# Kernel tuning notes

Measured on AMD Instinct MI355X. Metric: run time of the kernel, lower is better.

The kernel has to match this reference:

```python
import jax, jax.numpy as jnp
import numpy as np

DIM = 512
HEADS = 8
DIM_HEAD = 64
SCALE = DIM_HEAD ** -0.5


def setup_inputs() -> dict:
    key = jax.random.key(0)
    k1, k2, k3 = jax.random.split(key, 3)
    b, n = 2, 4096
    x = jax.random.normal(k1, (b, n, DIM), dtype=jnp.float32)
    ln_gamma = jnp.ones((DIM,), dtype=jnp.float32)
    ln_beta = jnp.zeros((DIM,), dtype=jnp.float32)
    w_qkv = jax.random.normal(k2, (DIM, 3 * HEADS * DIM_HEAD), dtype=jnp.float32) * (DIM ** -0.5)
    w_out = jax.random.normal(k3, (HEADS * DIM_HEAD, DIM), dtype=jnp.float32) * ((HEADS * DIM_HEAD) ** -0.5)
    b_out = jnp.zeros((DIM,), dtype=jnp.float32)
    return {"x": x, "ln_gamma": ln_gamma, "ln_beta": ln_beta,
            "w_qkv": w_qkv, "w_out": w_out, "b_out": b_out}


def reference(x, ln_gamma, ln_beta, w_qkv, w_out, b_out):
    # LayerNorm over last dim (eps matches torch default 1e-5)
    mu = jnp.mean(x, axis=-1, keepdims=True)
    var = jnp.mean(jnp.square(x - mu), axis=-1, keepdims=True)
    xn = (x - mu) * jax.lax.rsqrt(var + 1e-5) * ln_gamma + ln_beta

    b, n, _ = xn.shape
    qkv = xn @ w_qkv                                  # [b, n, 3*h*d]
    q, k, v = jnp.split(qkv, 3, axis=-1)
    # [b, n, h*d] -> [b, h, n, d]
    reshape = lambda t: t.reshape(b, n, HEADS, DIM_HEAD).transpose(0, 2, 1, 3)
    q, k, v = reshape(q), reshape(k), reshape(v)

    dots = jnp.einsum('bhid,bhjd->bhij', q, k) * SCALE  # [b, h, n, n]
    attn = jax.nn.softmax(dots, axis=-1)
    out = jnp.einsum('bhij,bhjd->bhid', attn, v)        # [b, h, n, d]
    out = out.transpose(0, 2, 1, 3).reshape(b, n, HEADS * DIM_HEAD)
    return out @ w_out + b_out
```

## Files before the change

kernel.cpp:

```cpp
#include <hip/hip_runtime.h>
#include <stdint.h>

#define NBATCH 2
#define NSEQ   4096
#define DIMF   512
#define HEADS  8
#define DHEAD  64
#define MTOK   (NBATCH*NSEQ)
#define NBH    (NBATCH*HEADS)

typedef __bf16 bf16x8 __attribute__((ext_vector_type(8)));
typedef float  f32x4  __attribute__((ext_vector_type(4)));
typedef short  short8v __attribute__((ext_vector_type(8)));

__device__ __forceinline__ unsigned short f2bf(float f) {
  unsigned x = __builtin_bit_cast(unsigned, f);
  x += 0x7fffu + ((x >> 16) & 1u);
  return (unsigned short)(x >> 16);
}

__device__ __forceinline__ void gld16(void* lds, const void* g) {
  __builtin_amdgcn_global_load_lds(
      (const __attribute__((address_space(1))) unsigned*)g,
      (__attribute__((address_space(3))) unsigned*)lds, 16, 0, 0);
}

__global__ __launch_bounds__(256) void ln_kernel(
    const float* __restrict__ x, const float* __restrict__ gamma,
    const float* __restrict__ beta, unsigned* __restrict__ xnb) {
  const int row = blockIdx.x;
  const int t = threadIdx.x;
  const float2 v = *(const float2*)(x + (size_t)row * DIMF + t * 2);
  float s1 = v.x + v.y;
  float s2 = v.x * v.x + v.y * v.y;
#pragma unroll
  for (int m = 1; m < 64; m <<= 1) { s1 += __shfl_xor(s1, m); s2 += __shfl_xor(s2, m); }
  __shared__ float ls1[4], ls2[4];
  const int w = t >> 6;
  if ((t & 63) == 0) { ls1[w] = s1; ls2[w] = s2; }
  __syncthreads();
  s1 = ls1[0] + ls1[1] + ls1[2] + ls1[3];
  s2 = ls2[0] + ls2[1] + ls2[2] + ls2[3];
  const float mu  = s1 * (1.0f / 512.0f);
  const float var = s2 * (1.0f / 512.0f) - mu * mu;
  const float rs  = 1.0f / sqrtf(var + 1e-5f);
  const float2 g2 = *(const float2*)(gamma + t * 2);
  const float2 b2 = *(const float2*)(beta + t * 2);
  const float a0 = (v.x - mu) * rs * g2.x + b2.x;
  const float a1 = (v.y - mu) * rs * g2.y + b2.y;
  xnb[(size_t)row * 256 + t] = (unsigned)f2bf(a0) | ((unsigned)f2bf(a1) << 16);
}

__global__ __launch_bounds__(256) void wprep_kernel(
    const float* __restrict__ wqkv, const float* __restrict__ wout,
    unsigned short* __restrict__ wqkvT, unsigned short* __restrict__ woT) {
  const int tid = blockIdx.x * 256 + threadIdx.x;
  if (tid < 512 * 1536) {
    const int c = tid % 1536, k = tid / 1536;
    wqkvT[c * 512 + k] = f2bf(wqkv[(size_t)k * 1536 + c]);
  } else {
    const int i = tid - 512 * 1536;
    const int c = i % 512, k = i / 512;
    woT[c * 512 + k] = f2bf(wout[(size_t)k * 512 + c]);
  }
}

template <int MODE>
__global__ __launch_bounds__(256, 2) void gemm_kernel(
    const unsigned short* __restrict__ A, const unsigned short* __restrict__ Bt,
    unsigned short* __restrict__ Qb, unsigned short* __restrict__ Kb,
    unsigned short* __restrict__ Vb,
    const float* __restrict__ bias, float* __restrict__ Cout, int Ncols) {
  __shared__ short Ab[2][128 * 32];
  __shared__ short Bb[2][128 * 32];
  const int tid = threadIdx.x;
  const int w = tid >> 6, l = tid & 63;
  const int g = l >> 4, c = l & 15;
  const int nbn = Ncols >> 7;
  const int mb = blockIdx.x / nbn, nb = blockIdx.x % nbn;
  const int m0 = mb * 128, n0 = nb * 128;
  const int wr = w >> 1, wc = w & 1;

  f32x4 acc[4][4] = {};

  auto STAGE = [&](int buf, int kt) {
    const int k0 = kt * 32;
#pragma unroll
    for (int j = 0; j < 2; ++j) {
      const int row = w * 32 + j * 16 + (l >> 2);
      const int gk = (l & 3) ^ ((row >> 1) & 3);
      gld16(&Ab[buf][(w * 32 + j * 16) * 32], A + (size_t)(m0 + row) * 512 + k0 + gk * 8);
      gld16(&Bb[buf][(w * 32 + j * 16) * 32], Bt + (size_t)(n0 + row) * 512 + k0 + gk * 8);
    }
  };

  STAGE(0, 0);
  __syncthreads();

  for (int kt = 0; kt < 16; ++kt) {
    const int buf = kt & 1;
    if (kt + 1 < 16) STAGE(buf ^ 1, kt + 1);
    bf16x8 af[4], bfr[4];
#pragma unroll
    for (int rt = 0; rt < 4; ++rt) {
      const int row = wr * 64 + rt * 16 + c;
      const int slot = g ^ ((row >> 1) & 3);
      af[rt] = __builtin_bit_cast(bf16x8, *(const short8v*)&Ab[buf][row * 32 + slot * 8]);
    }
#pragma unroll
    for (int nt = 0; nt < 4; ++nt) {
      const int row = wc * 64 + nt * 16 + c;
      const int slot = g ^ ((row >> 1) & 3);
      bfr[nt] = __builtin_bit_cast(bf16x8, *(const short8v*)&Bb[buf][row * 32 + slot * 8]);
    }
#pragma unroll
    for (int rt = 0; rt < 4; ++rt)
#pragma unroll
      for (int nt = 0; nt < 4; ++nt)
        acc[rt][nt] = __builtin_amdgcn_mfma_f32_16x16x32_bf16(af[rt], bfr[nt], acc[rt][nt], 0, 0, 0);
    __syncthreads();
  }

#pragma unroll
  for (int rt = 0; rt < 4; ++rt)
#pragma unroll
    for (int nt = 0; nt < 4; ++nt) {
      const int col = n0 + wc * 64 + nt * 16 + c;
#pragma unroll
      for (int r = 0; r < 4; ++r) {
        const int m = m0 + wr * 64 + rt * 16 + g * 4 + r;
        const float v = acc[rt][nt][r];
        if (MODE == 0) {
          const int sec = col >> 9, hh = (col >> 6) & 7, dh = col & 63;
          const int bh = (m >> 12) * 8 + hh, n = m & 4095;
          const size_t idx = (size_t)(bh * 4096 + n) * 64 + dh;
          if (sec == 0)      Qb[idx] = f2bf(v * 0.18033688011112042f);
          else if (sec == 1) Kb[idx] = f2bf(v);
          else               Vb[idx] = f2bf(v);
        } else {
          Cout[(size_t)m * 512 + col] = v + bias[col];
        }
      }
    }
}

__global__ __launch_bounds__(256) void vtrans_kernel(
    const unsigned short* __restrict__ Vb, unsigned short* __restrict__ Vtb) {
  __shared__ unsigned short tl[64][72];
  const int tid = threadIdx.x;
  const int bh = blockIdx.x >> 6, nt = blockIdx.x & 63;
  const int n0 = nt * 64;
  const unsigned short* src = Vb + ((size_t)bh * 4096 + n0) * 64;
#pragma unroll
  for (int h = 0; h < 2; ++h) {
    const int r = (tid >> 3) + h * 32;
    const int c0 = (tid & 7) * 8;
    *(short8v*)&tl[r][c0] = *(const short8v*)(src + r * 64 + c0);
  }
  __syncthreads();
#pragma unroll
  for (int h = 0; h < 2; ++h) {
    const int d = (tid >> 3) + h * 32;
    const int m0 = (tid & 7) * 8;
    unsigned short tmp[8];
#pragma unroll
    for (int i = 0; i < 8; ++i) tmp[i] = tl[m0 + i][d];
    *(short8v*)(Vtb + ((size_t)bh * 64 + d) * 4096 + n0 + m0) = *(const short8v*)&tmp[0];
  }
}

__global__ __launch_bounds__(256, 2) void attn_kernel(
    const unsigned short* __restrict__ Qb, const unsigned short* __restrict__ Kb,
    const unsigned short* __restrict__ Vtb, unsigned short* __restrict__ attnb) {
  __shared__ short Kbuf[2][64 * 64];
  __shared__ short Vbuf[2][64 * 64];
  __shared__ short PT[4][32 * 64];
  const int tid = threadIdx.x;
  const int w = tid >> 6, l = tid & 63;
  const int g = l >> 4, c = l & 15, c7 = l & 7;
  const int bh = blockIdx.x & 15, qb = blockIdx.x >> 4;
  const int q0 = qb * 128 + w * 32;
  const unsigned short* Qp = Qb + (size_t)(bh * 4096 + q0) * 64;
  const unsigned short* Kp = Kb + (size_t)bh * 4096 * 64;
  const unsigned short* Vp = Vtb + (size_t)bh * 64 * 4096;

  bf16x8 qf[2][2];
#pragma unroll
  for (int qt = 0; qt < 2; ++qt)
#pragma unroll
    for (int kk = 0; kk < 2; ++kk)
      qf[qt][kk] = __builtin_bit_cast(bf16x8,
          *(const short8v*)(Qp + (size_t)(qt * 16 + c) * 64 + kk * 32 + g * 8));

  short8v ones_s;
#pragma unroll
  for (int i = 0; i < 8; ++i) ones_s[i] = (short)0x3f80;
  const bf16x8 ones = __builtin_bit_cast(bf16x8, ones_s);

  f32x4 O[2][4] = {};
  f32x4 osum[2] = {};
  char* Pw = (char*)&PT[w][0];

  auto STAGEKV = [&](int buf, int t) {
    const int kv0 = t * 64;
#pragma unroll
    for (int j = 0; j < 2; ++j) {
      const int row = w * 16 + j * 8 + (l >> 3);
      const int gk = (l & 7) ^ (row & 7);
      gld16(&Kbuf[buf][(w * 16 + j * 8) * 64], Kp + (size_t)(kv0 + row) * 64 + gk * 8);
      gld16(&Vbuf[buf][(w * 16 + j * 8) * 64], Vp + (size_t)row * 4096 + kv0 + gk * 8);
    }
  };

  STAGEKV(0, 0);
  __syncthreads();

  for (int t = 0; t < 64; ++t) {
    const int buf = t & 1;
    if (t + 1 < 64) STAGEKV(buf ^ 1, t + 1);

#pragma unroll
    for (int kt = 0; kt < 4; ++kt) {
      const int krow = kt * 16 + c;
      bf16x8 kf0 = __builtin_bit_cast(bf16x8,
          *(const short8v*)&Kbuf[buf][krow * 64 + ((0 * 4 + g) ^ c7) * 8]);
      bf16x8 kf1 = __builtin_bit_cast(bf16x8,
          *(const short8v*)&Kbuf[buf][krow * 64 + ((1 * 4 + g) ^ c7) * 8]);
#pragma unroll
      for (int qt = 0; qt < 2; ++qt) {
        f32x4 S = {};
        S = __builtin_amdgcn_mfma_f32_16x16x32_bf16(kf0, qf[qt][0], S, 0, 0, 0);
        S = __builtin_amdgcn_mfma_f32_16x16x32_bf16(kf1, qf[qt][1], S, 0, 0, 0);
        const float p0 = exp2f(S[0]);
        const float p1 = exp2f(S[1]);
        const float p2 = exp2f(S[2]);
        const float p3 = exp2f(S[3]);
        unsigned u0, u1;
        asm("v_cvt_pk_bf16_f32 %0, %1, %2" : "=v"(u0) : "v"(p0), "v"(p1));
        asm("v_cvt_pk_bf16_f32 %0, %1, %2" : "=v"(u1) : "v"(p2), "v"(p3));
        *(uint2*)(Pw + (qt * 16 + c) * 128 + ((kt * 32 + g * 8) ^ (c7 * 16))) =
            make_uint2(u0, u1);
      }
    }

    bf16x8 vf[4][2];
#pragma unroll
    for (int nt = 0; nt < 4; ++nt) {
      const int vrow = nt * 16 + c;
#pragma unroll
      for (int kk = 0; kk < 2; ++kk)
        vf[nt][kk] = __builtin_bit_cast(bf16x8,
            *(const short8v*)&Vbuf[buf][vrow * 64 + (((kk * 4 + g) ^ c7) * 8)]);
    }
#pragma unroll
    for (int rt = 0; rt < 2; ++rt)
#pragma unroll
      for (int kk = 0; kk < 2; ++kk) {
        bf16x8 pa = __builtin_bit_cast(bf16x8,
            *(const short8v*)(Pw + (rt * 16 + c) * 128 + ((kk * 64 + g * 16) ^ (c7 * 16))));
        osum[rt] = __builtin_amdgcn_mfma_f32_16x16x32_bf16(pa, ones, osum[rt], 0, 0, 0);
#pragma unroll
        for (int nt = 0; nt < 4; ++nt)
          O[rt][nt] = __builtin_amdgcn_mfma_f32_16x16x32_bf16(pa, vf[nt][kk], O[rt][nt], 0, 0, 0);
      }
    __syncthreads();
  }

  float linv[2][4];
#pragma unroll
  for (int rt = 0; rt < 2; ++rt)
#pragma unroll
    for (int r = 0; r < 4; ++r) linv[rt][r] = 1.0f / osum[rt][r];

  const int tok0 = (bh >> 3) * 4096 + q0;
  const int col0 = (bh & 7) * 64;
#pragma unroll
  for (int rt = 0; rt < 2; ++rt)
#pragma unroll
    for (int nt = 0; nt < 4; ++nt)
#pragma unroll
      for (int r = 0; r < 4; ++r) {
        const int tok = tok0 + rt * 16 + g * 4 + r;
        attnb[(size_t)tok * 512 + col0 + nt * 16 + c] = f2bf(O[rt][nt][r] * linv[rt][r]);
      }
}

extern "C" void kernel_launch(void* const* d_in, const int* in_sizes, int n_in,
                              void* d_out, int out_size, void* d_ws, size_t ws_size,
                              hipStream_t stream) {
  (void)in_sizes; (void)n_in; (void)out_size; (void)ws_size;
  const float* x     = (const float*)d_in[0];
  const float* gamma = (const float*)d_in[1];
  const float* beta  = (const float*)d_in[2];
  const float* wqkv  = (const float*)d_in[3];
  const float* wout  = (const float*)d_in[4];
  const float* bout  = (const float*)d_in[5];
  float* out = (float*)d_out;

  char* ws = (char*)d_ws;
  size_t off = 0;
  auto alloc = [&](size_t bytes) {
    void* p = ws + off;
    off += (bytes + 255) & ~(size_t)255;
    return p;
  };
  unsigned*       xnb   = (unsigned*)alloc((size_t)MTOK * DIMF * 2);
  unsigned short* wqkvT = (unsigned short*)alloc((size_t)1536 * 512 * 2);
  unsigned short* woT   = (unsigned short*)alloc((size_t)512 * 512 * 2);
  unsigned short* Qbuf  = (unsigned short*)alloc((size_t)NBH * NSEQ * DHEAD * 2);
  unsigned short* Kb    = (unsigned short*)alloc((size_t)NBH * NSEQ * DHEAD * 2);
  unsigned short* Vtb   = (unsigned short*)alloc((size_t)NBH * NSEQ * DHEAD * 2);
  unsigned short* attnb = (unsigned short*)alloc((size_t)MTOK * DIMF * 2);
  unsigned short* Vb    = attnb;

  ln_kernel<<<dim3(MTOK), dim3(256), 0, stream>>>(x, gamma, beta, xnb);
  wprep_kernel<<<dim3(4096), dim3(256), 0, stream>>>(wqkv, wout, wqkvT, woT);
  gemm_kernel<0><<<dim3(64 * 12), dim3(256), 0, stream>>>(
      (const unsigned short*)xnb, wqkvT, Qbuf, Kb, Vb, nullptr, nullptr, 1536);
  vtrans_kernel<<<dim3(NBH * 64), dim3(256), 0, stream>>>(Vb, Vtb);
  attn_kernel<<<dim3(512), dim3(256), 0, stream>>>(Qbuf, Kb, Vtb, attnb);
  gemm_kernel<1><<<dim3(64 * 4), dim3(256), 0, stream>>>(
      attnb, woT, nullptr, nullptr, nullptr, bout, out, 512);
}
```

Baseline: 243.2 us.

## Split attention KV range into two chunks, use permlane swaps instead of LDS for P

The attention kernel now splits the key/value sequence into two halves handled by separate blocks (1024 blocks instead of 512), writing unnormalized fp32 partial outputs and row sums. A new combine kernel adds the two partials, normalizes and converts to bf16. The P matrix is no longer round-tripped through LDS: v_permlane32/16_swap rearrange the exp values in registers into the MFMA A-operand layout. Occupancy hint is raised to 4 blocks per CU and MFMA sections get raised priority. This adds an extra kernel launch and fp32 partial-buffer traffic in exchange for more parallelism and less LDS use.

```diff
diff --git a/kernel.cpp b/kernel.cpp
--- a/kernel.cpp
+++ b/kernel.cpp
@@ -12,6 +12,7 @@
 typedef __bf16 bf16x8 __attribute__((ext_vector_type(8)));
 typedef float  f32x4  __attribute__((ext_vector_type(4)));
 typedef short  short8v __attribute__((ext_vector_type(8)));
+typedef unsigned uint4v __attribute__((ext_vector_type(4)));
 
 __device__ __forceinline__ unsigned short f2bf(float f) {
   unsigned x = __builtin_bit_cast(unsigned, f);
@@ -169,16 +170,18 @@
   }
 }
 
-__global__ __launch_bounds__(256, 2) void attn_kernel(
+__global__ __launch_bounds__(256, 4) void attn_kernel(
     const unsigned short* __restrict__ Qb, const unsigned short* __restrict__ Kb,
-    const unsigned short* __restrict__ Vtb, unsigned short* __restrict__ attnb) {
+    const unsigned short* __restrict__ Vtb, float* __restrict__ Opart,
+    float* __restrict__ spart) {
   __shared__ short Kbuf[2][64 * 64];
   __shared__ short Vbuf[2][64 * 64];
-  __shared__ short PT[4][32 * 64];
   const int tid = threadIdx.x;
   const int w = tid >> 6, l = tid & 63;
   const int g = l >> 4, c = l & 15, c7 = l & 7;
-  const int bh = blockIdx.x & 15, qb = blockIdx.x >> 4;
+  const int bh = blockIdx.x & 15;
+  const int qb = (blockIdx.x >> 4) & 31;
+  const int chunk = blockIdx.x >> 9;
   const int q0 = qb * 128 + w * 32;
   const unsigned short* Qp = Qb + (size_t)(bh * 4096 + q0) * 64;
   const unsigned short* Kp = Kb + (size_t)bh * 4096 * 64;
@@ -199,10 +202,9 @@
 
   f32x4 O[2][4] = {};
   f32x4 osum[2] = {};
-  char* Pw = (char*)&PT[w][0];
 
   auto STAGEKV = [&](int buf, int t) {
-    const int kv0 = t * 64;
+    const int kv0 = (chunk * 32 + t) * 64;
 #pragma unroll
     for (int j = 0; j < 2; ++j) {
       const int row = w * 16 + j * 8 + (l >> 3);
@@ -215,10 +217,11 @@
   STAGEKV(0, 0);
   __syncthreads();
 
-  for (int t = 0; t < 64; ++t) {
+  for (int t = 0; t < 32; ++t) {
     const int buf = t & 1;
-    if (t + 1 < 64) STAGEKV(buf ^ 1, t + 1);
-
+    if (t + 1 < 32) STAGEKV(buf ^ 1, t + 1);
+
+    unsigned xu[2][4][2];
 #pragma unroll
     for (int kt = 0; kt < 4; ++kt) {
       const int krow = kt * 16 + c;
@@ -238,51 +241,77 @@
         unsigned u0, u1;
         asm("v_cvt_pk_bf16_f32 %0, %1, %2" : "=v"(u0) : "v"(p0), "v"(p1));
         asm("v_cvt_pk_bf16_f32 %0, %1, %2" : "=v"(u1) : "v"(p2), "v"(p3));
-        *(uint2*)(Pw + (qt * 16 + c) * 128 + ((kt * 32 + g * 8) ^ (c7 * 16))) =
-            make_uint2(u0, u1);
+        xu[qt][kt][0] = u0;
+        xu[qt][kt][1] = u1;
       }
     }
 
-    bf16x8 vf[4][2];
-#pragma unroll
-    for (int nt = 0; nt < 4; ++nt) {
-      const int vrow = nt * 16 + c;
-#pragma unroll
-      for (int kk = 0; kk < 2; ++kk)
-        vf[nt][kk] = __builtin_bit_cast(bf16x8,
+#pragma unroll
+    for (int kk = 0; kk < 2; ++kk) {
+      bf16x8 vf[4];
+#pragma unroll
+      for (int nt = 0; nt < 4; ++nt) {
+        const int vrow = nt * 16 + c;
+        vf[nt] = __builtin_bit_cast(bf16x8,
             *(const short8v*)&Vbuf[buf][vrow * 64 + (((kk * 4 + g) ^ c7) * 8)]);
-    }
-#pragma unroll
-    for (int rt = 0; rt < 2; ++rt)
-#pragma unroll
-      for (int kk = 0; kk < 2; ++kk) {
-        bf16x8 pa = __builtin_bit_cast(bf16x8,
-            *(const short8v*)(Pw + (rt * 16 + c) * 128 + ((kk * 64 + g * 16) ^ (c7 * 16))));
+      }
+#pragma unroll
+      for (int rt = 0; rt < 2; ++rt) {
+        unsigned a0 = xu[rt][2 * kk][0], a2 = xu[rt][2 * kk + 1][0];
+        asm("v_permlane32_swap_b32 %0, %1" : "+v"(a0), "+v"(a2));
+        asm("v_permlane16_swap_b32 %0, %1" : "+v"(a0), "+v"(a2));
+        unsigned a1 = xu[rt][2 * kk][1], a3 = xu[rt][2 * kk + 1][1];
+        asm("v_permlane32_swap_b32 %0, %1" : "+v"(a1), "+v"(a3));
+        asm("v_permlane16_swap_b32 %0, %1" : "+v"(a1), "+v"(a3));
+        uint4v av; av[0] = a0; av[1] = a1; av[2] = a2; av[3] = a3;
+        const bf16x8 pa = __builtin_bit_cast(bf16x8, av);
+        __builtin_amdgcn_s_setprio(1);
         osum[rt] = __builtin_amdgcn_mfma_f32_16x16x32_bf16(pa, ones, osum[rt], 0, 0, 0);
 #pragma unroll
         for (int nt = 0; nt < 4; ++nt)
-          O[rt][nt] = __builtin_amdgcn_mfma_f32_16x16x32_bf16(pa, vf[nt][kk], O[rt][nt], 0, 0, 0);
+          O[rt][nt] = __builtin_amdgcn_mfma_f32_16x16x32_bf16(pa, vf[nt], O[rt][nt], 0, 0, 0);
+        __builtin_amdgcn_s_setprio(0);
       }
+    }
     __syncthreads();
   }
 
-  float linv[2][4];
-#pragma unroll
-  for (int rt = 0; rt < 2; ++rt)
-#pragma unroll
-    for (int r = 0; r < 4; ++r) linv[rt][r] = 1.0f / osum[rt][r];
-
-  const int tok0 = (bh >> 3) * 4096 + q0;
-  const int col0 = (bh & 7) * 64;
-#pragma unroll
-  for (int rt = 0; rt < 2; ++rt)
+  float* Op = Opart + ((size_t)(chunk * 16 + bh) * 4096 + q0) * 64;
+#pragma unroll
+  for (int rt = 0; rt < 2; ++rt) {
 #pragma unroll
     for (int nt = 0; nt < 4; ++nt)
 #pragma unroll
-      for (int r = 0; r < 4; ++r) {
-        const int tok = tok0 + rt * 16 + g * 4 + r;
-        attnb[(size_t)tok * 512 + col0 + nt * 16 + c] = f2bf(O[rt][nt][r] * linv[rt][r]);
-      }
+      for (int r = 0; r < 4; ++r)
+        Op[(size_t)(rt * 16 + g * 4 + r) * 64 + nt * 16 + c] = O[rt][nt][r];
+    if (c == 0) {
+#pragma unroll
+      for (int r = 0; r < 4; ++r)
+        spart[(size_t)(chunk * 16 + bh) * 4096 + q0 + rt * 16 + g * 4 + r] = osum[rt][r];
+    }
+  }
+}
+
+__global__ __launch_bounds__(256) void combine_kernel(
+    const float* __restrict__ Opart, const float* __restrict__ spart,
+    unsigned short* __restrict__ attnb) {
+  const size_t CH = (size_t)16 * 4096 * 64;
+  const int gid = blockIdx.x * 256 + threadIdx.x;
+  const size_t i = (size_t)gid * 4;
+  const int d = (int)(i & 63);
+  const int bhq = (int)(i >> 6);
+  const f32x4 o0 = *(const f32x4*)(Opart + i);
+  const f32x4 o1 = *(const f32x4*)(Opart + CH + i);
+  const float inv = 1.0f / (spart[bhq] + spart[bhq + 16 * 4096]);
+  const int bh = bhq >> 12, q = bhq & 4095;
+  const int tok = (bh >> 3) * 4096 + q;
+  const int col = (bh & 7) * 64 + d;
+  unsigned u0, u1;
+  const float r0 = (o0[0] + o1[0]) * inv, r1 = (o0[1] + o1[1]) * inv;
+  const float r2 = (o0[2] + o1[2]) * inv, r3 = (o0[3] + o1[3]) * inv;
+  u0 = (unsigned)f2bf(r0) | ((unsigned)f2bf(r1) << 16);
+  u1 = (unsigned)f2bf(r2) | ((unsigned)f2bf(r3) << 16);
+  *(uint2*)(attnb + (size_t)tok * 512 + col) = make_uint2(u0, u1);
 }
 
 extern "C" void kernel_launch(void* const* d_in, const int* in_sizes, int n_in,
@@ -311,6 +340,8 @@
   unsigned short* Kb    = (unsigned short*)alloc((size_t)NBH * NSEQ * DHEAD * 2);
   unsigned short* Vtb   = (unsigned short*)alloc((size_t)NBH * NSEQ * DHEAD * 2);
   unsigned short* attnb = (unsigned short*)alloc((size_t)MTOK * DIMF * 2);
+  float*          Opart = (float*)alloc((size_t)2 * NBH * NSEQ * DHEAD * 4);
+  float*          spart = (float*)alloc((size_t)2 * NBH * NSEQ * 4);
   unsigned short* Vb    = attnb;
 
   ln_kernel<<<dim3(MTOK), dim3(256), 0, stream>>>(x, gamma, beta, xnb);
@@ -318,7 +349,8 @@
   gemm_kernel<0><<<dim3(64 * 12), dim3(256), 0, stream>>>(
       (const unsigned short*)xnb, wqkvT, Qbuf, Kb, Vb, nullptr, nullptr, 1536);
   vtrans_kernel<<<dim3(NBH * 64), dim3(256), 0, stream>>>(Vb, Vtb);
-  attn_kernel<<<dim3(512), dim3(256), 0, stream>>>(Qbuf, Kb, Vtb, attnb);
+  attn_kernel<<<dim3(1024), dim3(256), 0, stream>>>(Qbuf, Kb, Vtb, Opart, spart);
+  combine_kernel<<<dim3(4096), dim3(256), 0, stream>>>(Opart, spart, attnb);
   gemm_kernel<1><<<dim3(64 * 4), dim3(256), 0, stream>>>(
       attnb, woT, nullptr, nullptr, nullptr, bout, out, 512);
 }
```

After: 230.5 us. 5.3% less time.
